# Kernel optimization log

Hardware: AMD Instinct MI355X
Metric: run time of the kernel (lower is better)

## Reference

```python
import jax, jax.numpy as jnp
import numpy as np

N_HEADS = 3
DS_ITERS = 20
EPS = 1e-8
LN_EPS = 1e-5


def rmsnorm(x, w):
    rms = jnp.sqrt(jnp.mean(x * x, axis=-1, keepdims=True) + EPS)
    return x / rms * w


def layernorm(x, w, b):
    m = jnp.mean(x, axis=-1, keepdims=True)
    v = jnp.mean((x - m) ** 2, axis=-1, keepdims=True)
    return (x - m) / jnp.sqrt(v + LN_EPS) * w + b


def sinkhorn(m):
    # m: [b, t, n, n]; global max-shift then exp, 20 alternating row/col normalizations
    m = m - jnp.max(m, axis=(-2, -1), keepdims=True)
    m = jnp.exp(m)
    def body(_, m):
        m = m / (jnp.sum(m, axis=-1, keepdims=True) + EPS)
        m = m / (jnp.sum(m, axis=-2, keepdims=True) + EPS)
        return m
    return jax.lax.fori_loop(0, DS_ITERS, body, m)


def encoder_block(x, ln1_w, ln1_b, Wq, Wk, Wv, Wo, ln2_w, ln2_b, W1, W2):
    # Standard pre-norm ViT encoder block, bias=False, dropout inactive (eval)
    b, t, d = x.shape
    hd = d // N_HEADS
    h = layernorm(x, ln1_w, ln1_b)
    q = (h @ Wq).reshape(b, t, N_HEADS, hd)
    k = (h @ Wk).reshape(b, t, N_HEADS, hd)
    v = (h @ Wv).reshape(b, t, N_HEADS, hd)
    scores = jnp.einsum('bqhd,bkhd->bhqk', q, k) / jnp.sqrt(jnp.asarray(hd, x.dtype))
    attn = jax.nn.softmax(scores, axis=-1)
    o = jnp.einsum('bhqk,bkhd->bqhd', attn, v).reshape(b, t, d) @ Wo
    x = x + o
    h2 = layernorm(x, ln2_w, ln2_b)
    x = x + jax.nn.gelu(h2 @ W1) @ W2
    return x


def setup_inputs() -> dict:
    key = jax.random.key(0)
    ks = jax.random.split(key, 12)
    b, t, n, d = 32, 1024, 4, 192
    nd, mlp = n * d, 768
    std = 0.02
    x = jax.random.normal(ks[0], (b, t, n, d), dtype=jnp.float32)
    b_res = jnp.full((n, n), -10.0, dtype=jnp.float32)
    b_res = b_res.at[jnp.arange(n), jnp.arange(n)].set(0.0)
    return {
        'x': x,
        'norm_w': jnp.ones((nd,), jnp.float32),
        'phi_pre': std * jax.random.normal(ks[1], (nd, n), jnp.float32),
        'phi_post': std * jax.random.normal(ks[2], (nd, n), jnp.float32),
        'phi_res': std * jax.random.normal(ks[3], (nd, n * n), jnp.float32),
        'b_pre': jnp.full((n,), float(np.log(1.0 / (n - 1.0))), jnp.float32),
        'b_post': jnp.zeros((n,), jnp.float32),
        'b_res': b_res,
        'alpha_pre': jnp.asarray(0.001, jnp.float32),
        'alpha_post': jnp.asarray(0.001, jnp.float32),
        'alpha_res': jnp.asarray(0.001, jnp.float32),
        'ln1_w': jnp.ones((d,), jnp.float32),
        'ln1_b': jnp.zeros((d,), jnp.float32),
        'Wq': std * jax.random.normal(ks[4], (d, d), jnp.float32),
        'Wk': std * jax.random.normal(ks[5], (d, d), jnp.float32),
        'Wv': std * jax.random.normal(ks[6], (d, d), jnp.float32),
        'Wo': std * jax.random.normal(ks[7], (d, d), jnp.float32),
        'ln2_w': jnp.ones((d,), jnp.float32),
        'ln2_b': jnp.zeros((d,), jnp.float32),
        'W1': std * jax.random.normal(ks[8], (d, mlp), jnp.float32),
        'W2': std * jax.random.normal(ks[9], (mlp, d), jnp.float32),
    }


def reference(x, norm_w, phi_pre, phi_post, phi_res, b_pre, b_post, b_res,
              alpha_pre, alpha_post, alpha_res,
              ln1_w, ln1_b, Wq, Wk, Wv, Wo, ln2_w, ln2_b, W1, W2):
    b, t, n, d = x.shape
    streams = rmsnorm(x.reshape(b, t, n * d), norm_w)
    pre_tilde = alpha_pre * (streams @ phi_pre) + b_pre              # [b,t,n]
    post_tilde = alpha_post * (streams @ phi_post) + b_post         # [b,t,n]
    res_tilde = alpha_res * (streams @ phi_res) + b_res.reshape(1, 1, n * n)
    h_pre = jax.nn.sigmoid(pre_tilde)
    h_post = 2.0 * jax.nn.sigmoid(post_tilde)
    h_res = sinkhorn(res_tilde.reshape(b, t, n, n))                 # doubly stochastic
    x_res = jnp.einsum('btij,btjd->btid', h_res, x)
    x_in = jnp.einsum('btn,btnd->btd', h_pre, x)
    y = encoder_block(x_in, ln1_w, ln1_b, Wq, Wk, Wv, Wo, ln2_w, ln2_b, W1, W2)
    x_out = y[:, :, None, :] * h_post[..., None]
    return x_res + x_out
```

## Files before the change

kernel.cpp:

```cpp
#include <hip/hip_runtime.h>
#include <hip/hip_bf16.h>
#include <math.h>

#define BATCH 32
#define SEQ   1024
#define NS    4
#define DIM   192
#define ND    768
#define NH    3
#define HD    64
#define MLP   768
#define TOKENS (BATCH*SEQ)

typedef __bf16 bf16;
typedef bf16  bf16x8 __attribute__((ext_vector_type(8)));
typedef bf16  bf16x4 __attribute__((ext_vector_type(4)));
typedef float f32x4  __attribute__((ext_vector_type(4)));

#define MFMA16(a,b,c) __builtin_amdgcn_mfma_f32_16x16x32_bf16(a,b,c,0,0,0)
#define LOG2E 1.44269504088896f

#if defined(__has_builtin)
#if __has_builtin(__builtin_amdgcn_exp2f)
#define EXP2F(x) __builtin_amdgcn_exp2f(x)
#else
#define EXP2F(x) exp2f(x)
#endif
#else
#define EXP2F(x) exp2f(x)
#endif

__device__ inline float gelu_tanh(float x) {
    float x3 = x * x * x;
    return 0.5f * x * (1.0f + tanhf(0.7978845608028654f * (x + 0.044715f * x3)));
}

__global__ __launch_bounds__(256) void wprep_kernel(
    const float* __restrict__ Wq, const float* __restrict__ Wk,
    const float* __restrict__ Wv, const float* __restrict__ Wo,
    const float* __restrict__ W1, const float* __restrict__ W2,
    const float* __restrict__ nw, const float* __restrict__ ppre,
    const float* __restrict__ ppost, const float* __restrict__ pres,
    bf16* __restrict__ wqkv, bf16* __restrict__ wot,
    bf16* __restrict__ w1t, bf16* __restrict__ w2t, bf16* __restrict__ phiw)
{
    const int z = blockIdx.z;
    const int tid = blockIdx.x * 256 + threadIdx.x;
    if (z == 6) {
        if (tid >= 32 * 96) return;
        const int n = tid / 96, k8 = tid % 96;
        const int kch = k8 >> 2, quad = k8 & 3;
        const int ntile = n >> 4, nc = n & 15;
        bf16* d = phiw + ((size_t)(ntile * 24 + kch) * 64 + quad * 16 + nc) * 8;
#pragma unroll
        for (int e = 0; e < 8; e++) {
            const int k = k8 * 8 + e;
            float v;
            if      (n < 4)  v = ppre [k * 4  + n];
            else if (n < 8)  v = ppost[k * 4  + n - 4];
            else if (n < 24) v = pres [k * 16 + n - 8];
            else             v = 0.f;
            d[e] = (bf16)(nw[k] * v);
        }
        return;
    }
    const float* src; bf16* dst; int K, N; float scale = 1.f;
    switch (z) {
        case 0: src = Wq; dst = wqkv;            K = 192; N = 192;
                scale = 0.125f * LOG2E; break;
        case 1: src = Wk; dst = wqkv + 36864;    K = 192; N = 192; break;
        case 2: src = Wv; dst = wqkv + 73728;    K = 192; N = 192; break;
        case 3: src = Wo; dst = wot;             K = 192; N = 192; break;
        case 4: src = W1; dst = w1t;             K = 192; N = 768; break;
        default:src = W2; dst = w2t;             K = 768; N = 192; break;
    }
    const int K8 = K >> 3, KC = K >> 5;
    if (tid >= N * K8) return;
    const int n = tid / K8, k8 = tid % K8;
    const int kch = k8 >> 2, quad = k8 & 3;
    const int ntile = n >> 4, nc = n & 15;
    bf16* d = dst + ((size_t)(ntile * KC + kch) * 64 + quad * 16 + nc) * 8;
#pragma unroll
    for (int e = 0; e < 8; e++)
        d[e] = (bf16)(scale * src[(size_t)(k8 * 8 + e) * N + n]);
}

__global__ __launch_bounds__(64) void prep_kernel(
    const float* __restrict__ x, bf16* __restrict__ xb, float* __restrict__ rinv)
{
    const int tok = blockIdx.x, lane = threadIdx.x;
    const float* xt = x + (size_t)tok * ND;
    float4 xv[3];
    float ssq = 0.f;
#pragma unroll
    for (int r = 0; r < 3; r++) {
        xv[r] = ((const float4*)xt)[lane + 64 * r];
        ssq += xv[r].x*xv[r].x + xv[r].y*xv[r].y + xv[r].z*xv[r].z + xv[r].w*xv[r].w;
    }
#pragma unroll
    for (int off = 32; off; off >>= 1) ssq += __shfl_xor(ssq, off);
    if (lane == 0) rinv[tok] = rsqrtf(ssq / (float)ND + 1e-8f);
#pragma unroll
    for (int r = 0; r < 3; r++) {
        bf16x4 o = {(bf16)xv[r].x, (bf16)xv[r].y, (bf16)xv[r].z, (bf16)xv[r].w};
        *(bf16x4*)(xb + (size_t)tok * ND + 4 * (lane + 64 * r)) = o;
    }
}

__global__ __launch_bounds__(256) void dots_kernel(
    const bf16* __restrict__ xb, const bf16* __restrict__ phiw,
    const float* __restrict__ rinv, float* __restrict__ dots)
{
    const int tid = threadIdx.x, lane = tid & 63, w = tid >> 6;
    const int quad = lane >> 4, c = lane & 15;
    const int tok0 = blockIdx.x * 64 + w * 16;

    f32x4 acc0 = {0.f,0.f,0.f,0.f}, acc1 = {0.f,0.f,0.f,0.f};
    const bf16* arow = xb + (size_t)(tok0 + c) * ND + quad * 8;
    const bf16* bbase = phiw + lane * 8;
#pragma unroll 6
    for (int k0 = 0; k0 < ND; k0 += 32) {
        const int kch = k0 >> 5;
        bf16x8 af  = *(const bf16x8*)(arow + k0);
        bf16x8 bf0 = *(const bf16x8*)(bbase + (size_t)kch * 512);
        bf16x8 bf1 = *(const bf16x8*)(bbase + (size_t)(24 + kch) * 512);
        acc0 = MFMA16(af, bf0, acc0);
        acc1 = MFMA16(af, bf1, acc1);
    }
#pragma unroll
    for (int r = 0; r < 4; r++) {
        const int tok = tok0 + quad * 4 + r;
        const float s = rinv[tok];
        dots[(size_t)tok * 32 + c]      = acc0[r] * s;
        dots[(size_t)tok * 32 + 16 + c] = acc1[r] * s;
    }
}

__global__ __launch_bounds__(256) void sink_kernel(
    const float* __restrict__ dots, const float* __restrict__ b_pre,
    const float* __restrict__ b_post, const float* __restrict__ b_res,
    const float* __restrict__ a_pre, const float* __restrict__ a_post,
    const float* __restrict__ a_res,
    float* __restrict__ hgate, float* __restrict__ hpost)
{
    const int tok = blockIdx.x * 256 + threadIdx.x;
    const float* dt = dots + (size_t)tok * 32;
    float d[24];
#pragma unroll
    for (int i = 0; i < 6; i++) *(float4*)&d[i*4] = *(const float4*)(dt + i*4);

    const float apre = a_pre[0], apost = a_post[0], ares = a_res[0];
    float hpre[4], hpo[4], m[16];
#pragma unroll
    for (int i = 0; i < 4; i++) {
        hpre[i] = 1.f / (1.f + __expf(-(apre  * d[i]     + b_pre[i])));
        hpo[i]  = 2.f / (1.f + __expf(-(apost * d[4 + i] + b_post[i])));
    }
#pragma unroll
    for (int p = 0; p < 16; p++) m[p] = ares * d[8 + p] + b_res[p];

    float gm = m[0];
#pragma unroll
    for (int p = 1; p < 16; p++) gm = fmaxf(gm, m[p]);
#pragma unroll
    for (int p = 0; p < 16; p++) m[p] = __expf(m[p] - gm);

    for (int it = 0; it < 20; it++) {
#pragma unroll
        for (int i = 0; i < 4; i++) {
            const float inv = 1.f / (m[i*4+0] + m[i*4+1] + m[i*4+2] + m[i*4+3] + 1e-8f);
#pragma unroll
            for (int j = 0; j < 4; j++) m[i*4+j] *= inv;
        }
#pragma unroll
        for (int j = 0; j < 4; j++) {
            const float inv = 1.f / (m[0*4+j] + m[1*4+j] + m[2*4+j] + m[3*4+j] + 1e-8f);
#pragma unroll
            for (int i = 0; i < 4; i++) m[i*4+j] *= inv;
        }
    }

    float* hg = hgate + (size_t)tok * 20;
#pragma unroll
    for (int i = 0; i < 4; i++) *(float4*)(hg + i*4) = *(float4*)&m[i*4];
    *(float4*)(hg + 16) = *(float4*)hpre;
    *(float4*)(hpost + (size_t)tok * 4) = *(float4*)hpo;
}

__global__ __launch_bounds__(64) void mix_kernel(
    const bf16* __restrict__ xb, const float* __restrict__ hgate,
    const float* __restrict__ ln1_w, const float* __restrict__ ln1_b,
    float* __restrict__ xin, bf16* __restrict__ h1)
{
    const int tok = blockIdx.x, lane = threadIdx.x;
    __shared__ float ldsx[ND];

    const bf16* xt = xb + (size_t)tok * ND;
#pragma unroll
    for (int r = 0; r < 3; r++) {
        const bf16x4 v = *(const bf16x4*)(xt + 4 * (lane + 64 * r));
        float4 f = {(float)v[0], (float)v[1], (float)v[2], (float)v[3]};
        ((float4*)ldsx)[lane + 64 * r] = f;
    }

    const float* hg = hgate + (size_t)tok * 20 + 16;
    float hpre[4];
#pragma unroll
    for (int i = 0; i < 4; i++) hpre[i] = hg[i];

    __syncthreads();

    float xi[3];
#pragma unroll
    for (int r = 0; r < 3; r++) {
        const int d = lane + 64 * r;
        xi[r] = hpre[0]*ldsx[d] + hpre[1]*ldsx[DIM+d]
              + hpre[2]*ldsx[2*DIM+d] + hpre[3]*ldsx[3*DIM+d];
    }
    float sum = xi[0] + xi[1] + xi[2];
#pragma unroll
    for (int off = 32; off; off >>= 1) sum += __shfl_xor(sum, off);
    const float mean = sum / (float)DIM;
    float vs = (xi[0]-mean)*(xi[0]-mean) + (xi[1]-mean)*(xi[1]-mean) + (xi[2]-mean)*(xi[2]-mean);
#pragma unroll
    for (int off = 32; off; off >>= 1) vs += __shfl_xor(vs, off);
    const float inv = rsqrtf(vs / (float)DIM + 1e-5f);

    float* xint = xin + (size_t)tok * DIM;
    bf16*  ht   = h1  + (size_t)tok * DIM;
#pragma unroll
    for (int r = 0; r < 3; r++) {
        const int d = lane + 64 * r;
        xint[d] = xi[r];
        ht[d]   = (bf16)((xi[r] - mean) * inv * ln1_w[d] + ln1_b[d]);
    }
}

template<int EPI, int K>
__global__ __launch_bounds__(256) void gemm_bf(
    const bf16* __restrict__ A, const bf16* __restrict__ Bt,
    bf16* __restrict__ Cb, int N)
{
    const int tid = threadIdx.x, lane = tid & 63, w = tid >> 6;
    const int quad = lane >> 4, c = lane & 15;
    const int tok0 = blockIdx.y * 256 + w * 64;
    const int n0   = blockIdx.x * 64;
    const int KC   = K >> 5;

    f32x4 acc[4][4];
#pragma unroll
    for (int i = 0; i < 4; i++)
#pragma unroll
        for (int j = 0; j < 4; j++) acc[i][j] = (f32x4){0.f,0.f,0.f,0.f};

    const bf16* abase = A + (size_t)(tok0 + c) * K + quad * 8;
    const bf16* bbase = Bt + (size_t)(n0 >> 4) * KC * 512 + lane * 8;
#pragma unroll 2
    for (int k0 = 0; k0 < K; k0 += 32) {
        const int kch = k0 >> 5;
        bf16x8 af[4], bfr[4];
#pragma unroll
        for (int mt = 0; mt < 4; mt++)
            af[mt] = *(const bf16x8*)(abase + (size_t)mt * 16 * K + k0);
#pragma unroll
        for (int nt = 0; nt < 4; nt++)
            bfr[nt] = *(const bf16x8*)(bbase + (size_t)(nt * KC + kch) * 512);
#pragma unroll
        for (int mt = 0; mt < 4; mt++)
#pragma unroll
            for (int nt = 0; nt < 4; nt++)
                acc[mt][nt] = MFMA16(af[mt], bfr[nt], acc[mt][nt]);
    }

#pragma unroll
    for (int mt = 0; mt < 4; mt++)
#pragma unroll
        for (int r = 0; r < 4; r++) {
            const int row = tok0 + mt*16 + quad*4 + r;
#pragma unroll
            for (int nt = 0; nt < 4; nt++) {
                float v = acc[mt][nt][r];
                if (EPI == 2) v = gelu_tanh(v);
                Cb[(size_t)row * N + n0 + nt*16 + c] = (bf16)v;
            }
        }
}

__global__ __launch_bounds__(256) void gemm_wo_ln(
    const bf16* __restrict__ A, const bf16* __restrict__ Bt,
    const float* __restrict__ xin, const float* __restrict__ lw,
    const float* __restrict__ lb, float* __restrict__ x1, bf16* __restrict__ h2)
{
    const int tid = threadIdx.x, lane = tid & 63, w = tid >> 6;
    const int quad = lane >> 4, c = lane & 15;
    const int tok0 = blockIdx.x * 64 + w * 16;

    f32x4 acc[12];
#pragma unroll
    for (int j = 0; j < 12; j++) acc[j] = (f32x4){0.f,0.f,0.f,0.f};

    const bf16* abase = A + (size_t)(tok0 + c) * 192 + quad * 8;
    const bf16* bbase = Bt + lane * 8;
#pragma unroll 2
    for (int k0 = 0; k0 < 192; k0 += 32) {
        const int kch = k0 >> 5;
        bf16x8 af = *(const bf16x8*)(abase + k0);
#pragma unroll
        for (int nt = 0; nt < 12; nt++) {
            bf16x8 bfr = *(const bf16x8*)(bbase + (size_t)(nt * 6 + kch) * 512);
            acc[nt] = MFMA16(af, bfr, acc[nt]);
        }
    }

#pragma unroll
    for (int r = 0; r < 4; r++) {
        const int row = tok0 + quad*4 + r;
        float v[12], s = 0.f;
#pragma unroll
        for (int nt = 0; nt < 12; nt++) {
            v[nt] = acc[nt][r] + xin[(size_t)row * 192 + nt*16 + c];
            s += v[nt];
        }
#pragma unroll
        for (int off = 1; off < 16; off <<= 1) s += __shfl_xor(s, off);
        const float mean = s / 192.f;
        float vv = 0.f;
#pragma unroll
        for (int nt = 0; nt < 12; nt++) {
            const float d = v[nt] - mean;
            vv += d * d;
        }
#pragma unroll
        for (int off = 1; off < 16; off <<= 1) vv += __shfl_xor(vv, off);
        const float inv = rsqrtf(vv / 192.f + 1e-5f);
#pragma unroll
        for (int nt = 0; nt < 12; nt++) {
            const int col = nt*16 + c;
            x1[(size_t)row * 192 + col] = v[nt];
            h2[(size_t)row * 192 + col] = (bf16)((v[nt] - mean) * inv * lw[col] + lb[col]);
        }
    }
}

__global__ __launch_bounds__(256) void gemm_w2_final(
    const bf16* __restrict__ A, const bf16* __restrict__ Bt,
    const float* __restrict__ x1, const float* __restrict__ x,
    const float* __restrict__ hgate, const float* __restrict__ hpost,
    float* __restrict__ out)
{
    const int tid = threadIdx.x, lane = tid & 63, w = tid >> 6;
    const int quad = lane >> 4, c = lane & 15;
    const int tok0 = blockIdx.y * 256 + w * 64;
    const int n0   = blockIdx.x * 64;

    f32x4 acc[4][4];
#pragma unroll
    for (int i = 0; i < 4; i++)
#pragma unroll
        for (int j = 0; j < 4; j++) acc[i][j] = (f32x4){0.f,0.f,0.f,0.f};

    const bf16* abase = A + (size_t)(tok0 + c) * 768 + quad * 8;
    const bf16* bbase = Bt + (size_t)(n0 >> 4) * 24 * 512 + lane * 8;
#pragma unroll 2
    for (int k0 = 0; k0 < 768; k0 += 32) {
        const int kch = k0 >> 5;
        bf16x8 af[4], bfr[4];
#pragma unroll
        for (int mt = 0; mt < 4; mt++)
            af[mt] = *(const bf16x8*)(abase + (size_t)mt * 16 * 768 + k0);
#pragma unroll
        for (int nt = 0; nt < 4; nt++)
            bfr[nt] = *(const bf16x8*)(bbase + (size_t)(nt * 24 + kch) * 512);
#pragma unroll
        for (int mt = 0; mt < 4; mt++)
#pragma unroll
            for (int nt = 0; nt < 4; nt++)
                acc[mt][nt] = MFMA16(af[mt], bfr[nt], acc[mt][nt]);
    }

#pragma unroll
    for (int mt = 0; mt < 4; mt++)
#pragma unroll
        for (int r = 0; r < 4; r++) {
            const int row = tok0 + mt*16 + quad*4 + r;
            const float* hg = hgate + (size_t)row * 20;
            float hres[16];
#pragma unroll
            for (int p = 0; p < 16; p++) hres[p] = hg[p];
            const float4 hp = *(const float4*)(hpost + (size_t)row * 4);
            const float hpi[4] = {hp.x, hp.y, hp.z, hp.w};
            const float* xrow = x + (size_t)row * ND;
            float* orow = out + (size_t)row * ND;
#pragma unroll
            for (int nt = 0; nt < 4; nt++) {
                const int col = n0 + nt*16 + c;
                const float y = acc[mt][nt][r] + x1[(size_t)row * 192 + col];
                float xv[4];
#pragma unroll
                for (int j = 0; j < 4; j++) xv[j] = xrow[j * 192 + col];
#pragma unroll
                for (int i = 0; i < 4; i++) {
                    const float xr = hres[i*4+0]*xv[0] + hres[i*4+1]*xv[1]
                                   + hres[i*4+2]*xv[2] + hres[i*4+3]*xv[3];
                    orow[i * 192 + col] = xr + y * hpi[i];
                }
            }
        }
}

__global__ __launch_bounds__(256) void vtrans_kernel(
    const bf16* __restrict__ qkv, bf16* __restrict__ vt)
{
    __shared__ bf16 t[64][72];
    const int tid = threadIdx.x;
    const int bh = blockIdx.y, b = bh / NH, h = bh % NH;
    const int s0 = blockIdx.x * 64;

#pragma unroll
    for (int i = 0; i < 2; i++) {
        const int chunk = tid + 256 * i;
        const int srow = chunk >> 3, g = chunk & 7;
        *(uint4*)&t[srow][g * 8] =
            *(const uint4*)(qkv + (size_t)(b * SEQ + s0 + srow) * 576 + 384 + h * 64 + g * 8);
    }
    __syncthreads();
#pragma unroll
    for (int i = 0; i < 2; i++) {
        const int chunk = tid + 256 * i;
        const int d = chunk >> 3, sg = chunk & 7;
        bf16x8 v;
#pragma unroll
        for (int j = 0; j < 8; j++) v[j] = t[sg * 8 + j][d];
        *(bf16x8*)(vt + ((size_t)bh * HD + d) * SEQ + s0 + sg * 8) = v;
    }
}

__device__ __forceinline__ void attn_tile_body(
    int kt, bool pref,
    const bf16* __restrict__ kbase, const bf16* __restrict__ vbase,
    bf16* __restrict__ Pw, int quad, int c,
    const bf16x8 (&qf)[2][2],
    const bf16x8 (&kcur)[2][4], bf16x8 (&knxt)[2][4],
    f32x4 (&of)[2][4], float (&lst)[2][4])
{
    bf16x8 vf[2][4];
#pragma unroll
    for (int ch = 0; ch < 2; ch++)
#pragma unroll
        for (int dt = 0; dt < 4; dt++)
            vf[ch][dt] = *(const bf16x8*)(vbase + (size_t)(dt*16 + c) * SEQ
                                          + kt*64 + ch*32 + quad*8);
    if (pref) {
#pragma unroll
        for (int ch = 0; ch < 2; ch++)
#pragma unroll
            for (int nt = 0; nt < 4; nt++)
                knxt[ch][nt] = *(const bf16x8*)(kbase
                    + (size_t)((kt+1)*64 + nt*16 + c) * 576 + ch*32 + quad*8);
    }

    f32x4 sf[2][4];
#pragma unroll
    for (int mt = 0; mt < 2; mt++)
#pragma unroll
        for (int nt = 0; nt < 4; nt++) sf[mt][nt] = (f32x4){0.f, 0.f, 0.f, 0.f};
#pragma unroll
    for (int ch = 0; ch < 2; ch++)
#pragma unroll
        for (int mt = 0; mt < 2; mt++)
#pragma unroll
            for (int nt = 0; nt < 4; nt++)
                sf[mt][nt] = MFMA16(qf[mt][ch], kcur[ch][nt], sf[mt][nt]);

#pragma unroll
    for (int mt = 0; mt < 2; mt++)
#pragma unroll
        for (int r = 0; r < 4; r++) {
            float rs = 0.f;
#pragma unroll
            for (int nt = 0; nt < 4; nt++) {
                const float p = EXP2F(sf[mt][nt][r]);
                sf[mt][nt][r] = p;
                rs += p;
            }
            lst[mt][r] += rs;
        }

#pragma unroll
    for (int mt = 0; mt < 2; mt++)
#pragma unroll
        for (int nt = 0; nt < 4; nt++)
#pragma unroll
            for (int r = 0; r < 4; r++) {
                const int row = mt*16 + quad*4 + r;
                const int col = nt*16 + c;
                Pw[row*64 + (((col >> 3) ^ (row & 7)) * 8) + (col & 7)] =
                    (bf16)sf[mt][nt][r];
            }

#pragma unroll
    for (int ch = 0; ch < 2; ch++) {
        bf16x8 pf[2];
#pragma unroll
        for (int mt = 0; mt < 2; mt++) {
            const int row = mt*16 + c;
            pf[mt] = *(const bf16x8*)(Pw + row*64 + (((ch*4 + quad) ^ (c & 7)) * 8));
        }
#pragma unroll
        for (int mt = 0; mt < 2; mt++)
#pragma unroll
            for (int dt = 0; dt < 4; dt++)
                of[mt][dt] = MFMA16(pf[mt], vf[ch][dt], of[mt][dt]);
    }
}

__global__ __launch_bounds__(64) void attn_mfma(
    const bf16* __restrict__ qkv, const bf16* __restrict__ vt,
    bf16* __restrict__ obuf)
{
    __shared__ bf16 Pw[32 * 64];
    const int lane = threadIdx.x;
    const int quad = lane >> 4, c = lane & 15;
    const int bh = blockIdx.y, b = bh / NH, h = bh % NH;
    const int q0 = blockIdx.x * 32;

    const bf16* kbase = qkv + (size_t)b * SEQ * 576 + 192 + h * 64;
    const bf16* vbase = vt + (size_t)bh * HD * SEQ;

    bf16x8 qf[2][2];
#pragma unroll
    for (int mt = 0; mt < 2; mt++)
#pragma unroll
        for (int ch = 0; ch < 2; ch++)
            qf[mt][ch] = *(const bf16x8*)(qkv + (size_t)(b * SEQ + q0 + mt*16 + c) * 576
                                              + h * 64 + ch * 32 + quad * 8);

    f32x4 of[2][4];
    float lst[2][4];
#pragma unroll
    for (int mt = 0; mt < 2; mt++)
#pragma unroll
        for (int r = 0; r < 4; r++) lst[mt][r] = 0.f;
#pragma unroll
    for (int mt = 0; mt < 2; mt++)
#pragma unroll
        for (int dt = 0; dt < 4; dt++) of[mt][dt] = (f32x4){0.f, 0.f, 0.f, 0.f};

    bf16x8 kfA[2][4], kfB[2][4];
#pragma unroll
    for (int ch = 0; ch < 2; ch++)
#pragma unroll
        for (int nt = 0; nt < 4; nt++)
            kfA[ch][nt] = *(const bf16x8*)(kbase + (size_t)(nt*16 + c) * 576
                                           + ch * 32 + quad * 8);

#pragma unroll 1
    for (int kt2 = 0; kt2 < SEQ / 64; kt2 += 2) {
        attn_tile_body(kt2,     true,           kbase, vbase, Pw, quad, c,
                       qf, kfA, kfB, of, lst);
        attn_tile_body(kt2 + 1, kt2 + 2 < SEQ/64, kbase, vbase, Pw, quad, c,
                       qf, kfB, kfA, of, lst);
    }

#pragma unroll
    for (int mt = 0; mt < 2; mt++)
#pragma unroll
        for (int r = 0; r < 4; r++) {
            float s = lst[mt][r];
#pragma unroll
            for (int off = 1; off < 16; off <<= 1) s += __shfl_xor(s, off);
            const float inv = 1.0f / s;
            const size_t tok = (size_t)b * SEQ + q0 + mt*16 + quad*4 + r;
#pragma unroll
            for (int dt = 0; dt < 4; dt++)
                obuf[tok * DIM + h*64 + dt*16 + c] = (bf16)(of[mt][dt][r] * inv);
        }
}

extern "C" void kernel_launch(void* const* d_in, const int* in_sizes, int n_in,
                              void* d_out, int out_size, void* d_ws, size_t ws_size,
                              hipStream_t stream) {
    const float* x         = (const float*)d_in[0];
    const float* norm_w    = (const float*)d_in[1];
    const float* phi_pre   = (const float*)d_in[2];
    const float* phi_post  = (const float*)d_in[3];
    const float* phi_res   = (const float*)d_in[4];
    const float* b_pre     = (const float*)d_in[5];
    const float* b_post    = (const float*)d_in[6];
    const float* b_res     = (const float*)d_in[7];
    const float* alpha_pre = (const float*)d_in[8];
    const float* alpha_post= (const float*)d_in[9];
    const float* alpha_res = (const float*)d_in[10];
    const float* ln1_w     = (const float*)d_in[11];
    const float* ln1_b     = (const float*)d_in[12];
    const float* Wq        = (const float*)d_in[13];
    const float* Wk        = (const float*)d_in[14];
    const float* Wv        = (const float*)d_in[15];
    const float* Wo        = (const float*)d_in[16];
    const float* ln2_w     = (const float*)d_in[17];
    const float* ln2_b     = (const float*)d_in[18];
    const float* W1        = (const float*)d_in[19];
    const float* W2        = (const float*)d_in[20];

    float* out = (float*)d_out;
    float* ws  = (float*)d_ws;

    const size_t TBf = (size_t)TOKENS * DIM;
    float* xin   = ws;
    float* x1    = ws + TBf;
    float* hpost = ws + 2 * TBf;
    float* rinv  = hpost + 131072;
    float* hgate = rinv + 32768;
    bf16*  phiw  = (bf16*)(hgate + (size_t)TOKENS*20);
    bf16*  wqkv  = phiw + 24576;
    bf16*  wot   = wqkv + 110592;
    bf16*  w1t   = wot + 36864;
    bf16*  w2t   = w1t + 147456;
    float* regAC = (float*)(w2t + 147456);
    bf16*  xb    = (bf16*)regAC;
    bf16*  qkv   = (bf16*)regAC;
    bf16*  vt    = qkv + (size_t)TOKENS * 576;
    bf16*  gbuf  = (bf16*)regAC;
    float* regBD = regAC + 12582912;
    bf16*  h1    = (bf16*)regBD;
    bf16*  obuf  = h1;
    bf16*  h2    = h1 + TBf;
    float* dotsb = regBD + TBf / 2;

    wprep_kernel<<<dim3(72, 1, 7), 256, 0, stream>>>(
        Wq, Wk, Wv, Wo, W1, W2, norm_w, phi_pre, phi_post, phi_res,
        wqkv, wot, w1t, w2t, phiw);

    prep_kernel<<<TOKENS, 64, 0, stream>>>(x, xb, rinv);
    dots_kernel<<<TOKENS / 64, 256, 0, stream>>>(xb, phiw, rinv, dotsb);
    sink_kernel<<<TOKENS / 256, 256, 0, stream>>>(
        dotsb, b_pre, b_post, b_res, alpha_pre, alpha_post, alpha_res, hgate, hpost);
    mix_kernel<<<TOKENS, 64, 0, stream>>>(xb, hgate, ln1_w, ln1_b, xin, h1);

    gemm_bf<0, 192><<<dim3(576/64, TOKENS/256), 256, 0, stream>>>(h1, wqkv, qkv, 576);

    vtrans_kernel<<<dim3(SEQ/64, BATCH*NH), 256, 0, stream>>>(qkv, vt);

    attn_mfma<<<dim3(SEQ/32, BATCH*NH), 64, 0, stream>>>(qkv, vt, obuf);

    gemm_wo_ln<<<TOKENS/64, 256, 0, stream>>>(obuf, wot, xin, ln2_w, ln2_b, x1, h2);

    gemm_bf<2, 192><<<dim3(768/64, TOKENS/256), 256, 0, stream>>>(h2, w1t, gbuf, 768);

    gemm_w2_final<<<dim3(3, TOKENS/256), 256, 0, stream>>>(
        gbuf, w2t, x1, x, hgate, hpost, out);
}
```

Measured before the change: 527.8 us.

## Software-pipeline attention QK and PV phases with double-buffered P tile

Splits the attention tile body into QK/softmax and PV phases and skews them, so tile t's scores are computed while the P·V accumulation for tile t-1 runs, using two LDS buffers for P. This aims to hide LDS write-to-read latency and MFMA dependency stalls within the single-wave block. Separately, GELU's tanhf is replaced by an exp2-based tanh formula to cut transcendental cost. Risks are more register pressure from holding more fragments live and slightly different GELU rounding.

```diff
diff --git a/kernel.cpp b/kernel.cpp
--- a/kernel.cpp
+++ b/kernel.cpp
@@ -31,8 +31,9 @@
 #endif
 
 __device__ inline float gelu_tanh(float x) {
-    float x3 = x * x * x;
-    return 0.5f * x * (1.0f + tanhf(0.7978845608028654f * (x + 0.044715f * x3)));
+    float y = 0.7978845608028654f * (x + 0.044715f * x * x * x);
+    float t = 1.0f - 2.0f / (1.0f + EXP2F(2.0f * LOG2E * y));
+    return 0.5f * x * (1.0f + t);
 }
 
 __global__ __launch_bounds__(256) void wprep_kernel(
@@ -435,21 +436,36 @@
     }
 }
 
-__device__ __forceinline__ void attn_tile_body(
-    int kt, bool pref,
-    const bf16* __restrict__ kbase, const bf16* __restrict__ vbase,
-    bf16* __restrict__ Pw, int quad, int c,
-    const bf16x8 (&qf)[2][2],
-    const bf16x8 (&kcur)[2][4], bf16x8 (&knxt)[2][4],
-    f32x4 (&of)[2][4], float (&lst)[2][4])
-{
-    bf16x8 vf[2][4];
+__device__ __forceinline__ void attn_load_v(
+    int kt, const bf16* __restrict__ vbase, int quad, int c, bf16x8 (&vf)[2][4])
+{
 #pragma unroll
     for (int ch = 0; ch < 2; ch++)
 #pragma unroll
         for (int dt = 0; dt < 4; dt++)
             vf[ch][dt] = *(const bf16x8*)(vbase + (size_t)(dt*16 + c) * SEQ
                                           + kt*64 + ch*32 + quad*8);
+}
+
+__device__ __forceinline__ void attn_load_pf(
+    const bf16* __restrict__ PwPrev, int quad, int c, bf16x8 (&pf)[2][2])
+{
+#pragma unroll
+    for (int ch = 0; ch < 2; ch++)
+#pragma unroll
+        for (int mt = 0; mt < 2; mt++)
+            pf[ch][mt] = *(const bf16x8*)(PwPrev + (mt*16 + c)*64
+                                          + (((ch*4 + quad) ^ (c & 7)) * 8));
+}
+
+__device__ __forceinline__ void attn_qk_phase(
+    int kt, bool pref,
+    const bf16* __restrict__ kbase,
+    bf16* __restrict__ PwCur, int quad, int c,
+    const bf16x8 (&qf)[2][2],
+    const bf16x8 (&kcur)[2][4], bf16x8 (&knxt)[2][4],
+    float (&lst)[2][4])
+{
     if (pref) {
 #pragma unroll
         for (int ch = 0; ch < 2; ch++)
@@ -494,36 +510,36 @@
             for (int r = 0; r < 4; r++) {
                 const int row = mt*16 + quad*4 + r;
                 const int col = nt*16 + c;
-                Pw[row*64 + (((col >> 3) ^ (row & 7)) * 8) + (col & 7)] =
+                PwCur[row*64 + (((col >> 3) ^ (row & 7)) * 8) + (col & 7)] =
                     (bf16)sf[mt][nt][r];
             }
-
-#pragma unroll
-    for (int ch = 0; ch < 2; ch++) {
-        bf16x8 pf[2];
-#pragma unroll
-        for (int mt = 0; mt < 2; mt++) {
-            const int row = mt*16 + c;
-            pf[mt] = *(const bf16x8*)(Pw + row*64 + (((ch*4 + quad) ^ (c & 7)) * 8));
-        }
+}
+
+__device__ __forceinline__ void attn_pv_accum(
+    const bf16x8 (&pf)[2][2], const bf16x8 (&vf)[2][4], f32x4 (&of)[2][4])
+{
+#pragma unroll
+    for (int ch = 0; ch < 2; ch++)
 #pragma unroll
         for (int mt = 0; mt < 2; mt++)
 #pragma unroll
             for (int dt = 0; dt < 4; dt++)
-                of[mt][dt] = MFMA16(pf[mt], vf[ch][dt], of[mt][dt]);
-    }
+                of[mt][dt] = MFMA16(pf[ch][mt], vf[ch][dt], of[mt][dt]);
 }
 
 __global__ __launch_bounds__(64) void attn_mfma(
     const bf16* __restrict__ qkv, const bf16* __restrict__ vt,
     bf16* __restrict__ obuf)
 {
-    __shared__ bf16 Pw[32 * 64];
+    __shared__ bf16 PwBuf[2][32 * 64];
     const int lane = threadIdx.x;
     const int quad = lane >> 4, c = lane & 15;
     const int bh = blockIdx.y, b = bh / NH, h = bh % NH;
     const int q0 = blockIdx.x * 32;
 
+    bf16* Pw0 = PwBuf[0];
+    bf16* Pw1 = PwBuf[1];
+
     const bf16* kbase = qkv + (size_t)b * SEQ * 576 + 192 + h * 64;
     const bf16* vbase = vt + (size_t)bh * HD * SEQ;
 
@@ -553,13 +569,37 @@
         for (int nt = 0; nt < 4; nt++)
             kfA[ch][nt] = *(const bf16x8*)(kbase + (size_t)(nt*16 + c) * 576
                                            + ch * 32 + quad * 8);
+    attn_qk_phase(0, true, kbase, Pw0, quad, c, qf, kfA, kfB, lst);
 
 #pragma unroll 1
-    for (int kt2 = 0; kt2 < SEQ / 64; kt2 += 2) {
-        attn_tile_body(kt2,     true,           kbase, vbase, Pw, quad, c,
-                       qf, kfA, kfB, of, lst);
-        attn_tile_body(kt2 + 1, kt2 + 2 < SEQ/64, kbase, vbase, Pw, quad, c,
-                       qf, kfB, kfA, of, lst);
+    for (int t = 1; t <= 13; t += 2) {
+        {
+            bf16x8 vf[2][4], pf[2][2];
+            attn_load_v(t - 1, vbase, quad, c, vf);
+            attn_load_pf(Pw0, quad, c, pf);
+            attn_qk_phase(t, true, kbase, Pw1, quad, c, qf, kfB, kfA, lst);
+            attn_pv_accum(pf, vf, of);
+        }
+        {
+            bf16x8 vf[2][4], pf[2][2];
+            attn_load_v(t, vbase, quad, c, vf);
+            attn_load_pf(Pw1, quad, c, pf);
+            attn_qk_phase(t + 1, true, kbase, Pw0, quad, c, qf, kfA, kfB, lst);
+            attn_pv_accum(pf, vf, of);
+        }
+    }
+    {
+        bf16x8 vf[2][4], pf[2][2];
+        attn_load_v(14, vbase, quad, c, vf);
+        attn_load_pf(Pw0, quad, c, pf);
+        attn_qk_phase(15, false, kbase, Pw1, quad, c, qf, kfB, kfA, lst);
+        attn_pv_accum(pf, vf, of);
+    }
+    {
+        bf16x8 vf[2][4], pf[2][2];
+        attn_load_v(15, vbase, quad, c, vf);
+        attn_load_pf(Pw1, quad, c, pf);
+        attn_pv_accum(pf, vf, of);
     }
 
 #pragma unroll
```

Measured after the change: 522.7 us (median of 2 runs). No clear change (-1.0%).
